# Kernel optimization log

Measured on AMD Instinct MI355X. Metric: run time of the kernel, lower is better.

The kernel has to match this reference:

```python
import jax, jax.numpy as jnp
import numpy as np

COMMITMENT_COST = 1.0


def setup_inputs() -> dict:
    key = jax.random.key(0)
    k1, k2 = jax.random.split(key)
    B, D, H, W = 32, 256, 32, 32
    K = 1024
    z = jax.random.normal(k1, (B, D, H, W), dtype=jnp.float32)
    # torch init: uniform(-1/K, 1/K)
    codebook = jax.random.uniform(k2, (K, D), dtype=jnp.float32,
                                  minval=-1.0 / K, maxval=1.0 / K)
    return {"z": z, "codebook": codebook}


def reference(z, codebook):
    B, D, H, W = z.shape
    # (B, D, H, W) -> (B, H, W, D) -> (N, D)
    zp = jnp.transpose(z, (0, 2, 3, 1))
    zf = zp.reshape(-1, D)
    # squared euclidean distances (N, K): ||z||^2 + ||e||^2 - 2 z.e
    d = (jnp.sum(zf * zf, axis=1, keepdims=True)
         + jnp.sum(codebook * codebook, axis=1)
         - 2.0 * jnp.matmul(zf, codebook.T))
    idx = jnp.argmin(d, axis=1)                    # (N,)
    zq = codebook[idx].reshape(B, H, W, D)         # gather
    vq_loss = jnp.mean((jax.lax.stop_gradient(zq) - zp) ** 2)
    commitment_loss = jnp.mean((zq - jax.lax.stop_gradient(zp)) ** 2)
    loss = vq_loss + COMMITMENT_COST * commitment_loss
    # straight-through estimator
    zq_st = zp + jax.lax.stop_gradient(zq - zp)
    zq_out = jnp.transpose(zq_st, (0, 3, 1, 2))    # back to (B, D, H, W)
    indices = idx.reshape(B, H, W)
    return zq_out, indices, loss
```

## Files before the change

### kernel.cpp

```cpp
#include <hip/hip_runtime.h>

#define NPOS 32768
#define DDIM 256
#define KCODE 1024
#define HW 1024
#define BSTRIDE (256*1024)
#define OUT0_SIZE 8388608
#define OUT1_SIZE 32768

#define WS_ET   0
#define WS_ZN   262144
#define WS_EN   294912
#define WS_IDX  295936


__global__ void vq_zn(const float* __restrict__ z, float* __restrict__ zn) {
    int n = blockIdx.x * 256 + threadIdx.x;
    int b = n >> 10, hw = n & 1023;
    const float* zp = z + (size_t)b * BSTRIDE + hw;
    float half_s[2];
    #pragma unroll
    for (int h = 0; h < 2; ++h) {
        const float* p = zp + (size_t)(h * 128) * HW;
        float r[8];
        #pragma unroll
        for (int j = 0; j < 8; ++j) {
            float v = p[(size_t)j * HW];
            r[j] = __fmul_rn(v, v);
        }
        #pragma unroll
        for (int i = 8; i < 128; i += 8) {
            #pragma unroll
            for (int j = 0; j < 8; ++j) {
                float v = p[(size_t)(i + j) * HW];
                r[j] = __fadd_rn(r[j], __fmul_rn(v, v));
            }
        }
        half_s[h] = __fadd_rn(
            __fadd_rn(__fadd_rn(r[0], r[1]), __fadd_rn(r[2], r[3])),
            __fadd_rn(__fadd_rn(r[4], r[5]), __fadd_rn(r[6], r[7])));
    }
    zn[n] = __fadd_rn(half_s[0], half_s[1]);
}

__global__ void vq_en(const float* __restrict__ cb, float* __restrict__ en) {
    int k = blockIdx.x * 256 + threadIdx.x;
    const float* row = cb + (size_t)k * DDIM;
    float half_s[2];
    #pragma unroll
    for (int h = 0; h < 2; ++h) {
        const float* p = row + h * 128;
        float r[8];
        #pragma unroll
        for (int j = 0; j < 8; ++j) r[j] = __fmul_rn(p[j], p[j]);
        #pragma unroll
        for (int i = 8; i < 128; i += 8) {
            #pragma unroll
            for (int j = 0; j < 8; ++j)
                r[j] = __fadd_rn(r[j], __fmul_rn(p[i + j], p[i + j]));
        }
        half_s[h] = __fadd_rn(
            __fadd_rn(__fadd_rn(r[0], r[1]), __fadd_rn(r[2], r[3])),
            __fadd_rn(__fadd_rn(r[4], r[5]), __fadd_rn(r[6], r[7])));
    }
    en[k] = __fadd_rn(half_s[0], half_s[1]);
}

__global__ void vq_prep(const float* __restrict__ cb,
                        float* __restrict__ ws_f, float* __restrict__ loss_slot) {
    int k = blockIdx.x;
    int d = threadIdx.x;
    ws_f[WS_ET + d * KCODE + k] = cb[k * DDIM + d];
    if (blockIdx.x == 0 && threadIdx.x == 0) *loss_slot = 0.0f;
}

#define BM 64
#define BN 256
#define BK 16

__launch_bounds__(256, 2)
__global__ void vq_argmin(const float* __restrict__ z,
                          const float* __restrict__ ws_f,
                          int* __restrict__ idx_out) {
    __shared__ float As[BK][68];
    __shared__ float Bs[BK][260];
    __shared__ float enS[KCODE];

    const float* ET = ws_f + WS_ET;
    const float* znW = ws_f + WS_ZN;
    const float* enW = ws_f + WS_EN;

    int t  = threadIdx.x;
    int tx = t & 31;
    int ty = t >> 5;
    int n0 = blockIdx.x * BM;
    int b  = n0 >> 10, hw0 = n0 & 1023;
    const float* zb = z + (size_t)b * BSTRIDE + hw0;

    for (int i = t; i < KCODE; i += 256) enS[i] = enW[i];

    float znr[8];
    #pragma unroll
    for (int j = 0; j < 8; ++j) znr[j] = znW[n0 + ty * 8 + j];

    float m1[8];
    int   i1[8];
    #pragma unroll
    for (int j = 0; j < 8; ++j) { m1[j] = 1e30f; i1[j] = 0; }

    for (int kc = 0; kc < KCODE; kc += BN) {
        float acc[8][8];
        #pragma unroll
        for (int j = 0; j < 8; ++j)
            #pragma unroll
            for (int c = 0; c < 8; ++c) acc[j][c] = 0.0f;

        for (int d0 = 0; d0 < DDIM; d0 += BK) {
            __syncthreads();
            {
                int dk = t >> 4, p4 = (t & 15) << 2;
                *reinterpret_cast<float4*>(&As[dk][p4]) =
                    *reinterpret_cast<const float4*>(zb + (size_t)(d0 + dk) * HW + p4);
            }
            #pragma unroll
            for (int i = 0; i < 4; ++i) {
                int q = t + i * 256;
                int dk = q >> 6, k4 = (q & 63) << 2;
                *reinterpret_cast<float4*>(&Bs[dk][k4]) =
                    *reinterpret_cast<const float4*>(ET + (size_t)(d0 + dk) * KCODE + kc + k4);
            }
            __syncthreads();

            #pragma unroll
            for (int dk = 0; dk < BK; ++dk) {
                float4 a0 = *reinterpret_cast<const float4*>(&As[dk][ty * 8]);
                float4 a1 = *reinterpret_cast<const float4*>(&As[dk][ty * 8 + 4]);
                float4 b0 = *reinterpret_cast<const float4*>(&Bs[dk][tx * 8]);
                float4 b1 = *reinterpret_cast<const float4*>(&Bs[dk][tx * 8 + 4]);
                float a[8] = {a0.x, a0.y, a0.z, a0.w, a1.x, a1.y, a1.z, a1.w};
                float bb[8] = {b0.x, b0.y, b0.z, b0.w, b1.x, b1.y, b1.z, b1.w};
                #pragma unroll
                for (int j = 0; j < 8; ++j)
                    #pragma unroll
                    for (int c = 0; c < 8; ++c)
                        acc[j][c] = fmaf(a[j], bb[c], acc[j][c]);
            }
        }

        #pragma unroll
        for (int c = 0; c < 8; ++c) {
            int k = kc + tx * 8 + c;
            float ek = enS[k];
            #pragma unroll
            for (int j = 0; j < 8; ++j) {
                float t1 = __fadd_rn(znr[j], ek);
                float d  = __fsub_rn(t1, __fmul_rn(2.0f, acc[j][c]));
                if (d < m1[j]) { m1[j] = d; i1[j] = k; }
            }
        }
    }

    #pragma unroll
    for (int j = 0; j < 8; ++j) {
        float a1 = m1[j];
        int   ii = i1[j];
        #pragma unroll
        for (int off = 1; off < 32; off <<= 1) {
            float o1 = __shfl_xor(a1, off, 32);
            int   oi = __shfl_xor(ii, off, 32);
            if (o1 < a1 || (o1 == a1 && oi < ii)) { a1 = o1; ii = oi; }
        }
        if (tx == 0) idx_out[n0 + ty * 8 + j] = ii;
    }
}

__global__ void vq_gather(const float* __restrict__ z,
                          const float* __restrict__ cb,
                          const int* __restrict__ idx_ws,
                          float* __restrict__ out,
                          float* __restrict__ loss) {
    int n = blockIdx.x * 256 + threadIdx.x;
    int b = n >> 10, hw = n & 1023;
    int k = idx_ws[n];
    const float* e  = cb + (size_t)k * DDIM;
    const float* zp = z + (size_t)b * BSTRIDE + hw;
    float* op = out + (size_t)b * BSTRIDE + hw;
    float s = 0.0f;
    #pragma unroll 4
    for (int d = 0; d < DDIM; ++d) {
        float ev = e[d];
        float zv = zp[(size_t)d * HW];
        op[(size_t)d * HW] = ev;
        float df = ev - zv;
        s = fmaf(df, df, s);
    }
    out[OUT0_SIZE + n] = (float)k;

    #pragma unroll
    for (int off = 32; off > 0; off >>= 1) s += __shfl_down(s, off);
    __shared__ float red[4];
    int lane = threadIdx.x & 63, w = threadIdx.x >> 6;
    if (lane == 0) red[w] = s;
    __syncthreads();
    if (threadIdx.x == 0) {
        float tot = (red[0] + red[1] + red[2] + red[3]) * (2.0f / 8388608.0f);
        atomicAdd(loss, tot);
    }
}

extern "C" void kernel_launch(void* const* d_in, const int* in_sizes, int n_in,
                              void* d_out, int out_size, void* d_ws, size_t ws_size,
                              hipStream_t stream) {
    const float* z  = (const float*)d_in[0];
    const float* cb = (const float*)d_in[1];
    float* out  = (float*)d_out;
    float* ws_f = (float*)d_ws;
    int*   idx  = (int*)d_ws + WS_IDX;
    float* loss = out + OUT0_SIZE + OUT1_SIZE;

    vq_zn<<<NPOS / 256, 256, 0, stream>>>(z, ws_f + WS_ZN);
    vq_en<<<KCODE / 256, 256, 0, stream>>>(cb, ws_f + WS_EN);
    vq_prep<<<KCODE, 256, 0, stream>>>(cb, ws_f, loss);
    vq_argmin<<<NPOS / BM, 256, 0, stream>>>(z, ws_f, idx);
    vq_gather<<<NPOS / 256, 256, 0, stream>>>(z, cb, idx, out, loss);
}
```

Measured before the change: 365.9 us.

## Split argmin over codebook chunks with packed atomicMin and tiled codebook transpose

The argmin kernel now launches one block per (row tile, 256-code chunk) instead of looping over all codes. This raises the grid from 512 to 2048 blocks so more workgroups can run per CU, and the launch bound is raised to 4. Each block combines its partial minimum into a global 64-bit key (distance bits high, index low) with atomicMin, which vq_zn initialises along with the loss slot. The codebook transpose becomes a shared-memory tiled kernel, and the B tile in LDS gets a skewed layout to reduce bank conflicts. In exchange, z tiles are reloaded once per code chunk and the code adds global atomics.

After: 353.4 us. 1.04x faster.

```diff
diff --git a/kernel.cpp b/kernel.cpp
--- a/kernel.cpp
+++ b/kernel.cpp
@@ -8,13 +8,15 @@
 #define OUT0_SIZE 8388608
 #define OUT1_SIZE 32768
 
-#define WS_ET   0
-#define WS_ZN   262144
-#define WS_EN   294912
-#define WS_IDX  295936
-
-
-__global__ void vq_zn(const float* __restrict__ z, float* __restrict__ zn) {
+#define WS_ET     0
+#define WS_ZN     262144
+#define WS_EN     294912
+#define WS_PACKED 295936
+
+
+__global__ void vq_zn(const float* __restrict__ z, float* __restrict__ zn,
+                      unsigned long long* __restrict__ packed,
+                      float* __restrict__ loss_slot) {
     int n = blockIdx.x * 256 + threadIdx.x;
     int b = n >> 10, hw = n & 1023;
     const float* zp = z + (size_t)b * BSTRIDE + hw;
@@ -41,6 +43,8 @@
             __fadd_rn(__fadd_rn(r[4], r[5]), __fadd_rn(r[6], r[7])));
     }
     zn[n] = __fadd_rn(half_s[0], half_s[1]);
+    packed[n] = 0xFFFFFFFFFFFFFFFFull;
+    if (n == 0) *loss_slot = 0.0f;
 }
 
 __global__ void vq_en(const float* __restrict__ cb, float* __restrict__ en) {
@@ -66,97 +70,114 @@
     en[k] = __fadd_rn(half_s[0], half_s[1]);
 }
 
-__global__ void vq_prep(const float* __restrict__ cb,
-                        float* __restrict__ ws_f, float* __restrict__ loss_slot) {
-    int k = blockIdx.x;
-    int d = threadIdx.x;
-    ws_f[WS_ET + d * KCODE + k] = cb[k * DDIM + d];
-    if (blockIdx.x == 0 && threadIdx.x == 0) *loss_slot = 0.0f;
+__global__ void vq_trans(const float* __restrict__ cb, float* __restrict__ et) {
+    __shared__ float tile[64][65];
+    int k0 = (blockIdx.x & 15) * 64;
+    int d0 = (blockIdx.x >> 4) * 64;
+    int t = threadIdx.x;
+    #pragma unroll
+    for (int p = 0; p < 4; ++p) {
+        int r  = p * 16 + (t >> 4);
+        int c4 = (t & 15) * 4;
+        float4 v = *reinterpret_cast<const float4*>(
+            cb + (size_t)(k0 + r) * DDIM + d0 + c4);
+        tile[r][c4] = v.x; tile[r][c4+1] = v.y;
+        tile[r][c4+2] = v.z; tile[r][c4+3] = v.w;
+    }
+    __syncthreads();
+    #pragma unroll
+    for (int s = 0; s < 16; ++s) {
+        int dd = s * 4 + (t >> 6);
+        int kk = t & 63;
+        et[(size_t)(d0 + dd) * KCODE + k0 + kk] = tile[kk][dd];
+    }
 }
 
 #define BM 64
 #define BN 256
 #define BK 16
-
-__launch_bounds__(256, 2)
+#define BSKEW(k) ((k) + ((k) >> 3))
+
+__launch_bounds__(256, 4)
 __global__ void vq_argmin(const float* __restrict__ z,
                           const float* __restrict__ ws_f,
-                          int* __restrict__ idx_out) {
-    __shared__ float As[BK][68];
-    __shared__ float Bs[BK][260];
-    __shared__ float enS[KCODE];
-
-    const float* ET = ws_f + WS_ET;
+                          unsigned long long* __restrict__ packed) {
+    __shared__ float As[BK][64];
+    __shared__ float Bs[BK][288];
+
+    const float* ET  = ws_f + WS_ET;
     const float* znW = ws_f + WS_ZN;
     const float* enW = ws_f + WS_EN;
 
     int t  = threadIdx.x;
     int tx = t & 31;
     int ty = t >> 5;
-    int n0 = blockIdx.x * BM;
+    int bc = blockIdx.x & 3;
+    int bm = blockIdx.x >> 2;
+    int kc = bc * BN;
+    int n0 = bm * BM;
     int b  = n0 >> 10, hw0 = n0 & 1023;
     const float* zb = z + (size_t)b * BSTRIDE + hw0;
 
-    for (int i = t; i < KCODE; i += 256) enS[i] = enW[i];
-
     float znr[8];
     #pragma unroll
     for (int j = 0; j < 8; ++j) znr[j] = znW[n0 + ty * 8 + j];
+
+    float acc[8][8];
+    #pragma unroll
+    for (int j = 0; j < 8; ++j)
+        #pragma unroll
+        for (int c = 0; c < 8; ++c) acc[j][c] = 0.0f;
+
+    for (int d0 = 0; d0 < DDIM; d0 += BK) {
+        __syncthreads();
+        {
+            int dk = t >> 4, p4 = (t & 15) << 2;
+            float4 v = *reinterpret_cast<const float4*>(
+                zb + (size_t)(d0 + dk) * HW + p4);
+            As[dk][p4] = v.x; As[dk][p4+1] = v.y;
+            As[dk][p4+2] = v.z; As[dk][p4+3] = v.w;
+        }
+        #pragma unroll
+        for (int i = 0; i < 4; ++i) {
+            int q = t + i * 256;
+            int dk = q >> 6, m = q & 63;
+            float4 v = *reinterpret_cast<const float4*>(
+                ET + (size_t)(d0 + dk) * KCODE + kc + 4 * m);
+            int ph = BSKEW(4 * m);
+            *reinterpret_cast<float4*>(&Bs[dk][ph]) = v;
+        }
+        __syncthreads();
+
+        #pragma unroll
+        for (int dk = 0; dk < BK; ++dk) {
+            float4 a0 = *reinterpret_cast<const float4*>(&As[dk][ty * 8]);
+            float4 a1 = *reinterpret_cast<const float4*>(&As[dk][ty * 8 + 4]);
+            float4 b0 = *reinterpret_cast<const float4*>(&Bs[dk][9 * tx]);
+            float4 b1 = *reinterpret_cast<const float4*>(&Bs[dk][9 * tx + 4]);
+            float a[8]  = {a0.x, a0.y, a0.z, a0.w, a1.x, a1.y, a1.z, a1.w};
+            float bb[8] = {b0.x, b0.y, b0.z, b0.w, b1.x, b1.y, b1.z, b1.w};
+            #pragma unroll
+            for (int j = 0; j < 8; ++j)
+                #pragma unroll
+                for (int c = 0; c < 8; ++c)
+                    acc[j][c] = fmaf(a[j], bb[c], acc[j][c]);
+        }
+    }
 
     float m1[8];
     int   i1[8];
     #pragma unroll
     for (int j = 0; j < 8; ++j) { m1[j] = 1e30f; i1[j] = 0; }
-
-    for (int kc = 0; kc < KCODE; kc += BN) {
-        float acc[8][8];
-        #pragma unroll
-        for (int j = 0; j < 8; ++j)
-            #pragma unroll
-            for (int c = 0; c < 8; ++c) acc[j][c] = 0.0f;
-
-        for (int d0 = 0; d0 < DDIM; d0 += BK) {
-            __syncthreads();
-            {
-                int dk = t >> 4, p4 = (t & 15) << 2;
-                *reinterpret_cast<float4*>(&As[dk][p4]) =
-                    *reinterpret_cast<const float4*>(zb + (size_t)(d0 + dk) * HW + p4);
-            }
-            #pragma unroll
-            for (int i = 0; i < 4; ++i) {
-                int q = t + i * 256;
-                int dk = q >> 6, k4 = (q & 63) << 2;
-                *reinterpret_cast<float4*>(&Bs[dk][k4]) =
-                    *reinterpret_cast<const float4*>(ET + (size_t)(d0 + dk) * KCODE + kc + k4);
-            }
-            __syncthreads();
-
-            #pragma unroll
-            for (int dk = 0; dk < BK; ++dk) {
-                float4 a0 = *reinterpret_cast<const float4*>(&As[dk][ty * 8]);
-                float4 a1 = *reinterpret_cast<const float4*>(&As[dk][ty * 8 + 4]);
-                float4 b0 = *reinterpret_cast<const float4*>(&Bs[dk][tx * 8]);
-                float4 b1 = *reinterpret_cast<const float4*>(&Bs[dk][tx * 8 + 4]);
-                float a[8] = {a0.x, a0.y, a0.z, a0.w, a1.x, a1.y, a1.z, a1.w};
-                float bb[8] = {b0.x, b0.y, b0.z, b0.w, b1.x, b1.y, b1.z, b1.w};
-                #pragma unroll
-                for (int j = 0; j < 8; ++j)
-                    #pragma unroll
-                    for (int c = 0; c < 8; ++c)
-                        acc[j][c] = fmaf(a[j], bb[c], acc[j][c]);
-            }
-        }
-
-        #pragma unroll
-        for (int c = 0; c < 8; ++c) {
-            int k = kc + tx * 8 + c;
-            float ek = enS[k];
-            #pragma unroll
-            for (int j = 0; j < 8; ++j) {
-                float t1 = __fadd_rn(znr[j], ek);
-                float d  = __fsub_rn(t1, __fmul_rn(2.0f, acc[j][c]));
-                if (d < m1[j]) { m1[j] = d; i1[j] = k; }
-            }
+    #pragma unroll
+    for (int c = 0; c < 8; ++c) {
+        int k = kc + tx * 8 + c;
+        float ek = enW[k];
+        #pragma unroll
+        for (int j = 0; j < 8; ++j) {
+            float t1 = __fadd_rn(znr[j], ek);
+            float d  = __fsub_rn(t1, __fmul_rn(2.0f, acc[j][c]));
+            if (d < m1[j]) { m1[j] = d; i1[j] = k; }
         }
     }
 
@@ -170,18 +191,23 @@
             int   oi = __shfl_xor(ii, off, 32);
             if (o1 < a1 || (o1 == a1 && oi < ii)) { a1 = o1; ii = oi; }
         }
-        if (tx == 0) idx_out[n0 + ty * 8 + j] = ii;
+        if (tx == 0) {
+            unsigned long long key =
+                ((unsigned long long)__float_as_uint(a1) << 32) |
+                (unsigned long long)(unsigned)ii;
+            atomicMin(&packed[n0 + ty * 8 + j], key);
+        }
     }
 }
 
 __global__ void vq_gather(const float* __restrict__ z,
                           const float* __restrict__ cb,
-                          const int* __restrict__ idx_ws,
+                          const unsigned long long* __restrict__ packed,
                           float* __restrict__ out,
                           float* __restrict__ loss) {
     int n = blockIdx.x * 256 + threadIdx.x;
     int b = n >> 10, hw = n & 1023;
-    int k = idx_ws[n];
+    int k = (int)(unsigned)(packed[n] & 0xFFFFFFFFull);
     const float* e  = cb + (size_t)k * DDIM;
     const float* zp = z + (size_t)b * BSTRIDE + hw;
     float* op = out + (size_t)b * BSTRIDE + hw;
@@ -215,12 +241,13 @@
     const float* cb = (const float*)d_in[1];
     float* out  = (float*)d_out;
     float* ws_f = (float*)d_ws;
-    int*   idx  = (int*)d_ws + WS_IDX;
+    unsigned long long* packed =
+        (unsigned long long*)(ws_f + WS_PACKED);
     float* loss = out + OUT0_SIZE + OUT1_SIZE;
 
-    vq_zn<<<NPOS / 256, 256, 0, stream>>>(z, ws_f + WS_ZN);
+    vq_zn<<<NPOS / 256, 256, 0, stream>>>(z, ws_f + WS_ZN, packed, loss);
     vq_en<<<KCODE / 256, 256, 0, stream>>>(cb, ws_f + WS_EN);
-    vq_prep<<<KCODE, 256, 0, stream>>>(cb, ws_f, loss);
-    vq_argmin<<<NPOS / BM, 256, 0, stream>>>(z, ws_f, idx);
-    vq_gather<<<NPOS / 256, 256, 0, stream>>>(z, cb, idx, out, loss);
-}
+    vq_trans<<<64, 256, 0, stream>>>(cb, ws_f + WS_ET);
+    vq_argmin<<<(NPOS / BM) * (KCODE / BN), 256, 0, stream>>>(z, ws_f, packed);
+    vq_gather<<<NPOS / 256, 256, 0, stream>>>(z, cb, packed, out, loss);
+}
```
